# Kernel tuning notes

Measured on AMD Instinct MI355X. Metric: run time of the kernel, lower is better.

## Reference

```python
import jax, jax.numpy as jnp
import numpy as np

B, S, H = 2, 2048, 1024
NH, HD = 16, 64  # num_heads, head_dim


def setup_inputs() -> dict:
    key = jax.random.key(0)
    k1, k2, k3 = jax.random.split(key, 3)
    return {
        "hidden_states": jax.random.normal(k1, (B, S, H), dtype=jnp.float32),
        "attention_mask": jnp.zeros((B, S), dtype=jnp.float32),
        "w_qkv": jax.random.normal(k2, (3 * H, H), dtype=jnp.float32) * (1.0 / np.sqrt(H)),
        "b_qkv": jnp.zeros((3 * H,), dtype=jnp.float32),
        "w_out": jax.random.normal(k3, (H, H), dtype=jnp.float32) * (1.0 / np.sqrt(H)),
        "b_out": jnp.zeros((H,), dtype=jnp.float32),
    }


def reference(hidden_states, attention_mask, w_qkv, b_qkv, w_out, b_out):
    scale = HD ** -0.5
    qkv = hidden_states @ w_qkv.T + b_qkv          # [B,S,3H]
    qkv = qkv.reshape(B, S, 3, NH, HD)
    qkv = jnp.transpose(qkv, (2, 0, 3, 1, 4))      # [3,B,NH,S,HD]
    q, k, v = qkv[0], qkv[1], qkv[2]
    scores = jnp.einsum("bhqd,bhkd->bhqk", q, k) * scale
    # 2D additive mask broadcast to [B,1,1,S] as in torch unsqueeze path
    scores = scores + attention_mask[:, None, None, :]
    attn = jax.nn.softmax(scores, axis=-1)
    out = jnp.einsum("bhqk,bhkd->bhqd", attn, v)   # [B,NH,S,HD]
    out = jnp.transpose(out, (0, 2, 1, 3)).reshape(B, S, H)
    return out @ w_out.T + b_out
```

## Files before the change

### kernel.cpp

```cpp
#include <hip/hip_runtime.h>
#include <stdint.h>

typedef short bfrag __attribute__((ext_vector_type(8)));
typedef float f32x4 __attribute__((ext_vector_type(4)));

#define LOG2E 1.4426950408889634f

__device__ __forceinline__ ushort f2bf(float x){
  union { float f; uint32_t u; } c; c.f = x;
  uint32_t r = (c.u + 0x7fffu + ((c.u >> 16) & 1u)) >> 16;
  return (ushort)r;
}

__device__ __forceinline__ uint32_t cvt_pk_bf16(float lo, float hi){
  uint32_t r;
  asm("v_cvt_pk_bf16_f32 %0, %1, %2" : "=v"(r) : "v"(lo), "v"(hi));
  return r;
}

__device__ __forceinline__ void load_lds16(const void* g, void* l){
  __builtin_amdgcn_global_load_lds((const __attribute__((address_space(1))) void*)g,
                                   (__attribute__((address_space(3))) void*)l,
                                   16, 0, 0);
}

template<int CTRL>
__device__ __forceinline__ float dppf(float x){
  return __builtin_bit_cast(float, __builtin_amdgcn_update_dpp(
      0, __builtin_bit_cast(int, x), CTRL, 0xf, 0xf, true));
}
__device__ __forceinline__ float rowmax16(float x){
  x = fmaxf(x, dppf<0x128>(x));
  x = fmaxf(x, dppf<0x124>(x));
  x = fmaxf(x, dppf<0x122>(x));
  x = fmaxf(x, dppf<0x121>(x));
  return x;
}
__device__ __forceinline__ float rowsum16(float x){
  x += dppf<0x128>(x);
  x += dppf<0x124>(x);
  x += dppf<0x122>(x);
  x += dppf<0x121>(x);
  return x;
}

__global__ void cast_f32_bf16(const float* __restrict__ in, ushort* __restrict__ out, int n4){
  int i = blockIdx.x * blockDim.x + threadIdx.x;
  if (i < n4){
    float4 f = ((const float4*)in)[i];
    ushort4 u;
    u.x = f2bf(f.x); u.y = f2bf(f.y); u.z = f2bf(f.z); u.w = f2bf(f.w);
    ((ushort4*)out)[i] = u;
  }
}

__global__ __launch_bounds__(256)
void transpose_v(const ushort* __restrict__ v, ushort* __restrict__ vt){
  __shared__ ushort T[64*64];
  const int t = threadIdx.x;
  const int bh = blockIdx.y, s0 = blockIdx.x * 64;
  const ushort* vb = v + ((size_t)bh * 2048 + s0) * 64;
  ushort* vtb = vt + (size_t)bh * 64 * 2048 + s0;
#pragma unroll
  for (int i = 0; i < 2; i++){
    const int s = (t >> 3) + i*32, c = (t & 7) * 8;
    bfrag x = *(const bfrag*)(vb + (size_t)s * 64 + c);
    *(bfrag*)((char*)T + ((s*128 + c*2) ^ (((s >> 3) & 7) << 4))) = x;
  }
  __syncthreads();
#pragma unroll
  for (int i = 0; i < 2; i++){
    const int d = (t >> 3) + i*32, c = (t & 7) * 8;
    bfrag y;
#pragma unroll
    for (int j = 0; j < 8; j++){
      const int s = c + j;
      y[j] = *(const ushort*)((char*)T + ((s*128 + d*2) ^ (((s >> 3) & 7) << 4)));
    }
    *(bfrag*)(vtb + (size_t)d * 2048 + c) = y;
  }
}

template<int EPI>
__global__ __launch_bounds__(256)
void gemm_bt(const ushort* __restrict__ A, const ushort* __restrict__ B,
             const float* __restrict__ bias,
             ushort* __restrict__ dq, ushort* __restrict__ dk, ushort* __restrict__ dv,
             float* __restrict__ dout,
             int M, int N, int K)
{
  __shared__ ushort Alds[2][128*32];
  __shared__ ushort Blds[2][128*32];
  const int t = threadIdx.x;
  const int w = t >> 6, l = t & 63;
  const int lr = l & 15, lg = l >> 4;
  const int m0 = blockIdx.x * 128, n0 = blockIdx.y * 128;
  const int wm = (w >> 1) * 64, wn = (w & 1) * 64;

  f32x4 acc[4][4] = {};

  auto stage = [&](int buf, int kt){
#pragma unroll
    for (int i = 0; i < 2; i++){
      const int row = i*64 + w*16 + (l >> 2);
      const int ce  = (l & 3) * 8;
      load_lds16(A + (size_t)(m0 + row) * K + kt*32 + ce, &Alds[buf][(i*64 + w*16) * 32]);
      load_lds16(B + (size_t)(n0 + row) * K + kt*32 + ce, &Blds[buf][(i*64 + w*16) * 32]);
    }
  };

  const int nk = K >> 5;
  int cur = 0;
  stage(0, 0);
  __syncthreads();
  for (int kt = 0; kt < nk; kt++){
    if (kt + 1 < nk) stage(cur ^ 1, kt + 1);
    bfrag af[4], bfv[4];
#pragma unroll
    for (int f = 0; f < 4; f++){
      af[f]  = *(const bfrag*)&Alds[cur][(wm + f*16 + lr) * 32 + lg * 8];
      bfv[f] = *(const bfrag*)&Blds[cur][(wn + f*16 + lr) * 32 + lg * 8];
    }
#pragma unroll
    for (int mf = 0; mf < 4; mf++)
#pragma unroll
      for (int nf = 0; nf < 4; nf++)
        acc[mf][nf] = __builtin_amdgcn_mfma_f32_16x16x32_bf16(af[mf], bfv[nf], acc[mf][nf], 0, 0, 0);
    __syncthreads();
    cur ^= 1;
  }

#pragma unroll
  for (int mf = 0; mf < 4; mf++){
#pragma unroll
    for (int nf = 0; nf < 4; nf++){
      const int col = n0 + wn + nf*16 + lr;
      const float bs = bias[col];
#pragma unroll
      for (int r = 0; r < 4; r++){
        const int row = m0 + wm + mf*16 + lg*4 + r;
        const float vv = acc[mf][nf][r] + bs;
        if (EPI == 1){
          const int which = col >> 10;
          const int hd = col & 1023;
          const int bb = row >> 11, s = row & 2047;
          const int bh = (bb << 4) + (hd >> 6);
          ushort* dst = (which == 0) ? dq : (which == 1) ? dk : dv;
          dst[((size_t)bh * 2048 + s) * 64 + (hd & 63)] = f2bf(vv);
        } else {
          dout[(size_t)row * N + col] = vv;
        }
      }
    }
  }
}

__global__ __launch_bounds__(256)
void flash_attn(const ushort* __restrict__ q, const ushort* __restrict__ k,
                const ushort* __restrict__ vt, const float* __restrict__ mask,
                ushort* __restrict__ ao)
{
  __shared__ ushort Klds[2][64*64];
  __shared__ ushort Vlds[2][64*64];
  __shared__ ushort Plds[4][16*64];
  const int t = threadIdx.x;
  const int w = t >> 6, l = t & 63;
  const int lr = l & 15, lg = l >> 4;
  const int bh = blockIdx.y;
  const int b = bh >> 4, h = bh & 15;
  const int q0 = blockIdx.x * 64;
  const ushort* qb  = q  + (size_t)bh * 2048 * 64;
  const ushort* kb  = k  + (size_t)bh * 2048 * 64;
  const ushort* vtb = vt + (size_t)bh * 64 * 2048;
  const float* mb = mask + b * 2048;

  const int srow = t >> 3;
  const int spc  = (t & 7) * 16;

  auto stageKV = [&](int buf, int kv0){
#pragma unroll
    for (int i = 0; i < 2; i++){
      const int row = srow + i*32;
      const int off = spc ^ ((row & 7) << 4);
      load_lds16((const char*)(kb + (size_t)kv0 * 64) + row*128 + off,
                 (char*)&Klds[buf][0] + i*4096 + w*1024);
      load_lds16((const char*)vtb + (size_t)row * 4096 + kv0*2 + off,
                 (char*)&Vlds[buf][0] + i*4096 + w*1024);
    }
  };

  bfrag qf[2];
#pragma unroll
  for (int kf = 0; kf < 2; kf++){
    const int row = q0 + w*16 + lr;
    qf[kf] = *(const bfrag*)(qb + (size_t)row * 64 + kf*32 + lg*8);
  }

  float mrun[4], lsum[4];
  f32x4 oacc[4] = {};
#pragma unroll
  for (int r = 0; r < 4; r++){ mrun[r] = -1e30f; lsum[r] = 0.f; }

  const float SC2 = 0.125f * LOG2E;

  stageKV(0, 0);
  float mk[4], mkn[4] = {0.f, 0.f, 0.f, 0.f};
#pragma unroll
  for (int nf = 0; nf < 4; nf++) mk[nf] = mb[nf*16 + lr] * LOG2E;

  int cur = 0;
  for (int kv0 = 0; kv0 < 2048; kv0 += 64){
    __syncthreads();
    if (kv0 + 64 < 2048){
      stageKV(cur ^ 1, kv0 + 64);
#pragma unroll
      for (int nf = 0; nf < 4; nf++) mkn[nf] = mb[kv0 + 64 + nf*16 + lr] * LOG2E;
    }

    bfrag bk[4][2];
#pragma unroll
    for (int nf = 0; nf < 4; nf++)
#pragma unroll
      for (int kf = 0; kf < 2; kf++){
        const int row = nf*16 + lr;
        const int kbyte = kf*64 + lg*16;
        bk[nf][kf] = *(const bfrag*)((const char*)&Klds[cur][0] + row*128 + (kbyte ^ ((row & 7) << 4)));
      }
    f32x4 sa[4] = {};
#pragma unroll
    for (int nf = 0; nf < 4; nf++)
#pragma unroll
      for (int kf = 0; kf < 2; kf++)
        sa[nf] = __builtin_amdgcn_mfma_f32_16x16x32_bf16(qf[kf], bk[nf][kf], sa[nf], 0, 0, 0);

    float sc[4][4], mx4[4];
#pragma unroll
    for (int r = 0; r < 4; r++){
#pragma unroll
      for (int nf = 0; nf < 4; nf++) sc[r][nf] = sa[nf][r]*SC2 + mk[nf];
      mx4[r] = fmaxf(fmaxf(sc[r][0], sc[r][1]), fmaxf(sc[r][2], sc[r][3]));
    }

    const bool grew = (mx4[0] > mrun[0] + 8.f) | (mx4[1] > mrun[1] + 8.f) |
                      (mx4[2] > mrun[2] + 8.f) | (mx4[3] > mrun[3] + 8.f);
    if (__any(grew)){
#pragma unroll
      for (int r = 0; r < 4; r++){
        const float mnew = fmaxf(mrun[r], rowmax16(mx4[r]));
        const float c = __builtin_amdgcn_exp2f(mrun[r] - mnew);
        mrun[r] = mnew;
        lsum[r] *= c;
#pragma unroll
        for (int nf = 0; nf < 4; nf++) oacc[nf][r] *= c;
      }
    }

#pragma unroll
    for (int r = 0; r < 4; r++){
      const float p0 = __builtin_amdgcn_exp2f(sc[r][0] - mrun[r]);
      const float p1 = __builtin_amdgcn_exp2f(sc[r][1] - mrun[r]);
      const float p2 = __builtin_amdgcn_exp2f(sc[r][2] - mrun[r]);
      const float p3 = __builtin_amdgcn_exp2f(sc[r][3] - mrun[r]);
      lsum[r] += (p0 + p1) + (p2 + p3);
      const uint32_t w01 = cvt_pk_bf16(p0, p1);
      const uint32_t w23 = cvt_pk_bf16(p2, p3);
      const int prow = lg*4 + r;
      const int sw = (prow & 7) << 4;
      char* pbase = (char*)&Plds[w][0] + prow*128;
      *(ushort*)(pbase + ((lr*2      ) ^ sw)) = (ushort)w01;
      *(ushort*)(pbase + ((lr*2 + 32 ) ^ sw)) = (ushort)(w01 >> 16);
      *(ushort*)(pbase + ((lr*2 + 64 ) ^ sw)) = (ushort)w23;
      *(ushort*)(pbase + ((lr*2 + 96 ) ^ sw)) = (ushort)(w23 >> 16);
    }

    bfrag bv[4][2], ap[2];
#pragma unroll
    for (int nf = 0; nf < 4; nf++)
#pragma unroll
      for (int kf = 0; kf < 2; kf++){
        const int d = nf*16 + lr;
        const int kbyte = kf*64 + lg*16;
        bv[nf][kf] = *(const bfrag*)((const char*)&Vlds[cur][0] + d*128 + (kbyte ^ ((d & 7) << 4)));
      }
#pragma unroll
    for (int kf = 0; kf < 2; kf++){
      const int kbyte = kf*64 + lg*16;
      ap[kf] = *(const bfrag*)((const char*)&Plds[w][0] + lr*128 + (kbyte ^ ((lr & 7) << 4)));
    }
#pragma unroll
    for (int nf = 0; nf < 4; nf++)
#pragma unroll
      for (int kf = 0; kf < 2; kf++)
        oacc[nf] = __builtin_amdgcn_mfma_f32_16x16x32_bf16(ap[kf], bv[nf][kf], oacc[nf], 0, 0, 0);

#pragma unroll
    for (int nf = 0; nf < 4; nf++) mk[nf] = mkn[nf];
    cur ^= 1;
  }

#pragma unroll
  for (int r = 0; r < 4; r++){
    const float inv = 1.f / rowsum16(lsum[r]);
#pragma unroll
    for (int nf = 0; nf < 4; nf++){
      const int grow = b*2048 + q0 + w*16 + lg*4 + r;
      const int col = h*64 + nf*16 + lr;
      ao[(size_t)grow * 1024 + col] = f2bf(oacc[nf][r] * inv);
    }
  }
}

extern "C" void kernel_launch(void* const* d_in, const int* in_sizes, int n_in,
                              void* d_out, int out_size, void* d_ws, size_t ws_size,
                              hipStream_t stream)
{
  (void)in_sizes; (void)n_in; (void)out_size; (void)ws_size;
  const float* hs   = (const float*)d_in[0];
  const float* mask = (const float*)d_in[1];
  const float* wqkv = (const float*)d_in[2];
  const float* bqkv = (const float*)d_in[3];
  const float* wout = (const float*)d_in[4];
  const float* bout = (const float*)d_in[5];
  float* out = (float*)d_out;

  char* ws = (char*)d_ws;
  ushort* hs_bf = (ushort*)(ws);
  ushort* w1_bf = (ushort*)(ws + 8388608);
  ushort* w2_bf = (ushort*)(ws + 14680064);
  ushort* q_bf  = (ushort*)(ws + 16777216);
  ushort* k_bf  = (ushort*)(ws + 25165824);
  ushort* v_bf  = (ushort*)(ws + 33554432);
  ushort* vt_bf = (ushort*)(ws + 41943040);
  ushort* ao_bf = (ushort*)(ws + 50331648);

  cast_f32_bf16<<<4096, 256, 0, stream>>>(hs,   hs_bf, 4194304/4);
  cast_f32_bf16<<<3072, 256, 0, stream>>>(wqkv, w1_bf, 3145728/4);
  cast_f32_bf16<<<1024, 256, 0, stream>>>(wout, w2_bf, 1048576/4);

  gemm_bt<1><<<dim3(32, 24), 256, 0, stream>>>(hs_bf, w1_bf, bqkv,
                                               q_bf, k_bf, v_bf, nullptr,
                                               4096, 3072, 1024);
  transpose_v<<<dim3(32, 32), 256, 0, stream>>>(v_bf, vt_bf);
  flash_attn<<<dim3(32, 32), 256, 0, stream>>>(q_bf, k_bf, vt_bf, mask, ao_bf);
  gemm_bt<2><<<dim3(32, 8), 256, 0, stream>>>(ao_bf, w2_bf, bout,
                                              nullptr, nullptr, nullptr, out,
                                              4096, 1024, 1024);
}
```

Measured before the change: 147.2 us.

## Merge cast kernels and widen flash-attention blocks to 128 query rows

Three separate f32-to-bf16 cast launches are replaced by one kernel that writes all three buffers contiguously into the workspace, removing two launches. Flash attention now runs 512 threads (8 waves) per block covering 128 query rows. Each K/V tile staged in shared memory is therefore reused by twice as many queries, and each thread issues one async load per tile instead of two. This halves the grid to 512 blocks, which may lower occupancy or leave CUs idle. It also depends on the unseen wave-indexed code still lining up with 8 waves.

After: 136.0 us. -7.6%, faster.

```diff
diff --git a/kernel.cpp b/kernel.cpp
--- a/kernel.cpp
+++ b/kernel.cpp
@@ -44,14 +44,16 @@
   return x;
 }
 
-__global__ void cast_f32_bf16(const float* __restrict__ in, ushort* __restrict__ out, int n4){
-  int i = blockIdx.x * blockDim.x + threadIdx.x;
-  if (i < n4){
-    float4 f = ((const float4*)in)[i];
-    ushort4 u;
-    u.x = f2bf(f.x); u.y = f2bf(f.y); u.z = f2bf(f.z); u.w = f2bf(f.w);
-    ((ushort4*)out)[i] = u;
-  }
+__global__ void cast_all(const float* __restrict__ hs, const float* __restrict__ wqkv,
+                         const float* __restrict__ wout, ushort* __restrict__ out){
+  const int i = blockIdx.x * blockDim.x + threadIdx.x;
+  float4 f;
+  if (i < 1048576)       f = ((const float4*)hs)[i];
+  else if (i < 1835008)  f = ((const float4*)wqkv)[i - 1048576];
+  else                   f = ((const float4*)wout)[i - 1835008];
+  ushort4 u;
+  u.x = f2bf(f.x); u.y = f2bf(f.y); u.z = f2bf(f.z); u.w = f2bf(f.w);
+  ((ushort4*)out)[i] = u;
 }
 
 __global__ __launch_bounds__(256)
@@ -155,20 +157,20 @@
   }
 }
 
-__global__ __launch_bounds__(256)
+__global__ __launch_bounds__(512, 4)
 void flash_attn(const ushort* __restrict__ q, const ushort* __restrict__ k,
                 const ushort* __restrict__ vt, const float* __restrict__ mask,
                 ushort* __restrict__ ao)
 {
   __shared__ ushort Klds[2][64*64];
   __shared__ ushort Vlds[2][64*64];
-  __shared__ ushort Plds[4][16*64];
+  __shared__ ushort Plds[8][16*64];
   const int t = threadIdx.x;
   const int w = t >> 6, l = t & 63;
   const int lr = l & 15, lg = l >> 4;
   const int bh = blockIdx.y;
   const int b = bh >> 4, h = bh & 15;
-  const int q0 = blockIdx.x * 64;
+  const int q0 = blockIdx.x * 128;
   const ushort* qb  = q  + (size_t)bh * 2048 * 64;
   const ushort* kb  = k  + (size_t)bh * 2048 * 64;
   const ushort* vtb = vt + (size_t)bh * 64 * 2048;
@@ -178,15 +180,11 @@
   const int spc  = (t & 7) * 16;
 
   auto stageKV = [&](int buf, int kv0){
-#pragma unroll
-    for (int i = 0; i < 2; i++){
-      const int row = srow + i*32;
-      const int off = spc ^ ((row & 7) << 4);
-      load_lds16((const char*)(kb + (size_t)kv0 * 64) + row*128 + off,
-                 (char*)&Klds[buf][0] + i*4096 + w*1024);
-      load_lds16((const char*)vtb + (size_t)row * 4096 + kv0*2 + off,
-                 (char*)&Vlds[buf][0] + i*4096 + w*1024);
-    }
+    const int off = spc ^ ((srow & 7) << 4);
+    load_lds16((const char*)(kb + (size_t)kv0 * 64) + srow*128 + off,
+               (char*)&Klds[buf][0] + w*1024);
+    load_lds16((const char*)vtb + (size_t)srow * 4096 + kv0*2 + off,
+               (char*)&Vlds[buf][0] + w*1024);
   };
 
   bfrag qf[2];
@@ -333,15 +331,13 @@
   ushort* vt_bf = (ushort*)(ws + 41943040);
   ushort* ao_bf = (ushort*)(ws + 50331648);
 
-  cast_f32_bf16<<<4096, 256, 0, stream>>>(hs,   hs_bf, 4194304/4);
-  cast_f32_bf16<<<3072, 256, 0, stream>>>(wqkv, w1_bf, 3145728/4);
-  cast_f32_bf16<<<1024, 256, 0, stream>>>(wout, w2_bf, 1048576/4);
+  cast_all<<<8192, 256, 0, stream>>>(hs, wqkv, wout, (ushort*)ws);
 
   gemm_bt<1><<<dim3(32, 24), 256, 0, stream>>>(hs_bf, w1_bf, bqkv,
                                                q_bf, k_bf, v_bf, nullptr,
                                                4096, 3072, 1024);
   transpose_v<<<dim3(32, 32), 256, 0, stream>>>(v_bf, vt_bf);
-  flash_attn<<<dim3(32, 32), 256, 0, stream>>>(q_bf, k_bf, vt_bf, mask, ao_bf);
+  flash_attn<<<dim3(16, 32), 512, 0, stream>>>(q_bf, k_bf, vt_bf, mask, ao_bf);
   gemm_bt<2><<<dim3(32, 8), 256, 0, stream>>>(ao_bf, w2_bf, bout,
                                               nullptr, nullptr, nullptr, out,
                                               4096, 1024, 1024);
```
